# Kernel optimization log

Hardware: AMD Instinct MI355X
Metric: run time of the kernel (lower is better)

## Reference

```python
import jax, jax.numpy as jnp
import numpy as np
import math

B, S, D, H, L, K = 4, 2048, 256, 8, 2, 3  # batch, seq, dim, heads, MTA layers, conv kernel
HS = D // H
EPS = 1e-6


def layer_norm(x, g, b):
    m = jnp.mean(x, axis=-1, keepdims=True)
    v = jnp.mean((x - m) ** 2, axis=-1, keepdims=True)
    return (x - m) * jax.lax.rsqrt(v + EPS) * g + b


def temporal_encoder(x, W, b):
    # x: [B,S,D]; W: [L,K,D,D] (WIO), b: [L,D]. Stack of kernel-3 'SAME' Conv1d, GELU between.
    for i in range(L):
        x = jax.lax.conv_general_dilated(
            x, W[i], window_strides=(1,), padding=[(1, 1)],
            dimension_numbers=("NWC", "WIO", "NWC")) + b[i]
        if i < L - 1:
            x = jax.nn.gelu(x)
    return x


def setup_inputs() -> dict:
    key = jax.random.key(0)
    ks = jax.random.split(key, 10)
    w = lambda k, shape: jax.random.normal(k, shape, jnp.float32) * 0.02
    return {
        "x": jax.random.normal(ks[0], (B, S, D), jnp.float32),
        "ln1_g": jnp.ones((D,), jnp.float32), "ln1_b": jnp.zeros((D,), jnp.float32),
        "Wq": w(ks[1], (L, K, D, D)), "bq": jnp.zeros((L, D), jnp.float32),
        "Wk": w(ks[2], (L, K, D, D)), "bk": jnp.zeros((L, D), jnp.float32),
        "Wv": w(ks[3], (L, K, D, D)), "bv": jnp.zeros((L, D), jnp.float32),
        "ln2_g": jnp.ones((D,), jnp.float32), "ln2_b": jnp.zeros((D,), jnp.float32),
        "Wo1": w(ks[4], (D, D)), "bo1": jnp.zeros((D,), jnp.float32),
        "Wo2": w(ks[5], (D, D)), "bo2": jnp.zeros((D,), jnp.float32),
        "mask": jax.random.randint(ks[6], (B, S), 0, 2).astype(jnp.int32),
    }


def reference(x, ln1_g, ln1_b, Wq, bq, Wk, bk, Wv, bv, ln2_g, ln2_b, Wo1, bo1, Wo2, bo2, mask):
    b_, s_ = x.shape[0], x.shape[1]
    h = layer_norm(x, ln1_g, ln1_b)
    q = temporal_encoder(h, Wq, bq).reshape(b_, s_, H, HS)
    k = temporal_encoder(h, Wk, bk).reshape(b_, s_, H, HS)
    v = temporal_encoder(h, Wv, bv).reshape(b_, s_, H, HS)
    # attention scores [B,H,S,S]
    scores = jnp.einsum("bqhd,bkhd->bhqk", q, k) / math.sqrt(HS)
    m = mask[:, None, None, :].astype(scores.dtype)  # [B,1,1,S]
    scores = scores + (1.0 - m) * (-1e30)
    probs = jax.nn.softmax(scores, axis=-1)
    attn = jnp.einsum("bhqk,bkhd->bqhd", probs, v).reshape(b_, s_, D)
    residual = x + attn  # dropout p=0
    o = layer_norm(residual, ln2_g, ln2_b)
    o = jax.nn.gelu(o @ Wo1 + bo1)  # 1x1 Conv1D == per-token linear
    o = o @ Wo2 + bo2 + residual
    return o
```

## Files before the change

### kernel.cpp

```cpp
#include <hip/hip_runtime.h>
#include <hip/hip_bf16.h>
#include <math.h>

#define BB 4
#define SS 2048
#define DD 256
#define HH 8
#define HSZ 32

typedef __attribute__((ext_vector_type(8))) short short8;
typedef __attribute__((ext_vector_type(4))) float f32x4;

__device__ __forceinline__ void gload_lds16(const void* g, void* l) {
    __builtin_amdgcn_global_load_lds((const unsigned int*)g, (unsigned int*)l,
                                     16, 0, 0);
}

__device__ __forceinline__ float exp2_hw(float x) {
    float r;
    asm("v_exp_f32 %0, %1" : "=v"(r) : "v"(x));
    return r;
}

__device__ __forceinline__ unsigned int perm_pack(float a, float b, unsigned int sel) {
    unsigned int r;
    asm("v_perm_b32 %0, %1, %2, %3"
        : "=v"(r)
        : "v"(__float_as_uint(b)), "v"(__float_as_uint(a)), "s"(sel));
    return r;
}

__device__ __forceinline__ float gelu_f(float x) {
    float x3 = x * x * x;
    float z = 0.7978845608028654f * fmaf(0.044715f, x3, x);
    float e = __expf(2.0f * z);
    float t = 1.0f - 2.0f / (e + 1.0f);
    return 0.5f * x * (1.0f + t);
}

__device__ __forceinline__ unsigned short f2bf(float f) {
    unsigned int u = __float_as_uint(f);
    u = (u + 0x7fffu + ((u >> 16) & 1u)) >> 16;
    return (unsigned short)u;
}

template<bool HASRES>
__device__ __forceinline__ void ln_wave_body(
    int t, int lane,
    const float* __restrict__ x, const float* __restrict__ addin,
    const float* __restrict__ g, const float* __restrict__ bvec,
    float* __restrict__ resid_out, unsigned short* __restrict__ oln_bf)
{
    const int base = t * DD + lane * 4;
    float4 v4 = *(const float4*)&x[base];
    if (HASRES) {
        float4 a4 = *(const float4*)&addin[base];
        v4.x += a4.x; v4.y += a4.y; v4.z += a4.z; v4.w += a4.w;
        *(float4*)&resid_out[base] = v4;
    }
    float s = (v4.x + v4.y) + (v4.z + v4.w);
    #pragma unroll
    for (int o = 1; o < 64; o <<= 1) s += __shfl_xor(s, o);
    float mean = s * (1.0f / 256.0f);
    float dx = v4.x - mean, dy = v4.y - mean, dz = v4.z - mean, dw = v4.w - mean;
    float q = (dx * dx + dy * dy) + (dz * dz + dw * dw);
    #pragma unroll
    for (int o = 1; o < 64; o <<= 1) q += __shfl_xor(q, o);
    float r = rsqrtf(q * (1.0f / 256.0f) + 1e-6f);
    const float4 g4 = *(const float4*)&g[lane * 4];
    const float4 b4 = *(const float4*)&bvec[lane * 4];
    ushort4 o4;
    o4.x = f2bf(dx * r * g4.x + b4.x);
    o4.y = f2bf(dy * r * g4.y + b4.y);
    o4.z = f2bf(dz * r * g4.z + b4.z);
    o4.w = f2bf(dw * r * g4.w + b4.w);
    *(ushort4*)&oln_bf[base] = o4;
}

__global__ __launch_bounds__(256) void prep_kernel(
    const float* __restrict__ Wq, const float* __restrict__ Wk,
    const float* __restrict__ Wv, const float* __restrict__ Wo1,
    const float* __restrict__ Wo2, unsigned short* __restrict__ wt,
    const float* __restrict__ x, const float* __restrict__ ln1g,
    const float* __restrict__ ln1b, unsigned short* __restrict__ h_bf,
    const int* __restrict__ mask, float* __restrict__ maskf)
{
    if (blockIdx.x < 1280) {
        const int WCp = 3 * DD * DD;
        const int WMp = DD * DD;
        const float* src; unsigned short* dst; int R, rel;
        int i = blockIdx.x;
        if (i < 1152) {
            int seg = i / 192; rel = i % 192; R = 768;
            src = seg == 0 ? Wq : seg == 1 ? Wq + WCp : seg == 2 ? Wk :
                  seg == 3 ? Wk + WCp : seg == 4 ? Wv : Wv + WCp;
            dst = wt + (size_t)seg * WCp;
        } else {
            int j = i - 1152; int seg = j / 64; rel = j % 64; R = 256;
            src = seg == 0 ? Wo1 : Wo2;
            dst = wt + (size_t)6 * WCp + (size_t)seg * WMp;
        }
        __shared__ unsigned short t[32][33];
        const int tx = threadIdx.x & 31, ty = threadIdx.x >> 5;
        const int r0 = (rel / 8) * 32, c0 = (rel % 8) * 32;
        #pragma unroll
        for (int j = 0; j < 32; j += 8)
            t[ty + j][tx] = f2bf(src[(r0 + ty + j) * 256 + c0 + tx]);
        __syncthreads();
        #pragma unroll
        for (int j = 0; j < 32; j += 8)
            dst[(size_t)(c0 + ty + j) * R + r0 + tx] = t[tx][ty + j];
    } else if (blockIdx.x < 3328) {
        const int wv = threadIdx.x >> 6, lane = threadIdx.x & 63;
        ln_wave_body<false>((blockIdx.x - 1280) * 4 + wv, lane,
                            x, nullptr, ln1g, ln1b, nullptr, h_bf);
    } else {
        const float M_ON  = -8.0f * 1.4426950408889634f;
        const float M_OFF = -1.442695e30f;
        int i = (blockIdx.x - 3328) * 1024 + threadIdx.x * 4;
        int4 m4 = *(const int4*)&mask[i];
        float4 f4;
        f4.x = m4.x ? M_ON : M_OFF;
        f4.y = m4.y ? M_ON : M_OFF;
        f4.z = m4.z ? M_ON : M_OFF;
        f4.w = m4.w ? M_ON : M_OFF;
        *(float4*)&maskf[i] = f4;
    }
}

__global__ __launch_bounds__(256, 3) void convdual_kernel(
    const unsigned short* __restrict__ in,
    const unsigned short* __restrict__ W0a, const unsigned short* __restrict__ W0b,
    const unsigned short* __restrict__ W0c,
    const unsigned short* __restrict__ W1a, const unsigned short* __restrict__ W1b,
    const unsigned short* __restrict__ W1c,
    const float* __restrict__ ba, const float* __restrict__ bb,
    const float* __restrict__ bc,
    unsigned short* __restrict__ oQ, unsigned short* __restrict__ oK,
    unsigned short* __restrict__ oV, int S)
{
    constexpr int LDW = 264;
    __shared__ __align__(16) unsigned short stage[36 * LDW];
    __shared__ __align__(16) unsigned short wbuf[2][8192];

    unsigned short* const inter = stage;

    const int set = blockIdx.x % 3;
    const int tile = blockIdx.x / 3;
    const unsigned short* W0 = set == 0 ? W0a : (set == 1 ? W0b : W0c);
    const unsigned short* W1 = set == 0 ? W1a : (set == 1 ? W1b : W1c);
    const float* bias         = set == 0 ? ba  : (set == 1 ? bb  : bc);
    unsigned short* outp      = set == 0 ? oQ  : (set == 1 ? oK  : oV);

    const int tid = threadIdx.x;
    const int lane = tid & 63, wv = tid >> 6;
    const int lm = lane & 15, lq = lane >> 4;
    const int tpb = S / 32;
    const int b = tile / tpb;
    const int s0 = (tile % tpb) * 32;
    const int NC = S / 32;
    const int c = s0 >> 5;

    for (int i = tid; i < 36 * 32; i += 256) {
        int r = i >> 5, c8 = (i & 31) << 3;
        int s = s0 + r - 2;
        int4 val = make_int4(0, 0, 0, 0);
        if (s >= 0 && s < S)
            val = *(const int4*)&in[(size_t)(b * S + s) * 256 + c8];
        *(int4*)&stage[r * LDW + c8] = val;
    }

    const int n0 = wv * 64;

    const char* wsrc0[4];
    const char* wsrc1[4];
    char* wdst[4];
    {
        const unsigned int Lb = (unsigned int)(wv * 4096 + lane * 16);
        #pragma unroll
        for (int j = 0; j < 4; ++j) {
            unsigned int L = Lb + j * 1024u;
            unsigned int SL = L ^ (((L >> 7) & 7u) << 4);
            unsigned int so = (SL >> 6) * 1536u + (SL & 63u);
            wsrc0[j] = (const char*)W0 + so;
            wsrc1[j] = (const char*)W1 + so;
            wdst[j] = (char*)wbuf + (wv * 4096 + j * 1024);
        }
    }
    unsigned int boff[4];
    #pragma unroll
    for (int nt = 0; nt < 4; ++nt) {
        unsigned int och = (unsigned int)(n0 + nt * 16 + lm);
        unsigned int R = och * 64u + (unsigned int)lq * 16u;
        boff[nt] = R ^ (((R >> 7) & 7u) << 4);
    }

    __syncthreads();

    {
        f32x4 acc[3][4];
        #pragma unroll
        for (int mt = 0; mt < 3; ++mt)
            #pragma unroll
            for (int nt = 0; nt < 4; ++nt) acc[mt][nt] = (f32x4){0.f, 0.f, 0.f, 0.f};

        #pragma unroll
        for (int j = 0; j < 4; ++j) gload_lds16(wsrc0[j],       wdst[j]);
        #pragma unroll
        for (int j = 0; j < 4; ++j) gload_lds16(wsrc0[j] + 64,  wdst[j] + 16384);

        short8 a0c, a1c, a2c;
        {
            const int icc0 = lq * 8;
            int r20 = 32 + lm; r20 = r20 > 35 ? 35 : r20;
            a0c = *(const short8*)&stage[lm * LDW + icc0];
            a1c = *(const short8*)&stage[(16 + lm) * LDW + icc0];
            a2c = *(const short8*)&stage[r20 * LDW + icc0];
        }

        #pragma unroll
        for (int it = 0; it < 24; ++it) {
            if (it < 23) asm volatile("s_waitcnt vmcnt(4)" ::: "memory");
            else         asm volatile("s_waitcnt vmcnt(0)" ::: "memory");
            __builtin_amdgcn_sched_barrier(0);

            const char* wb = (const char*)wbuf + ((it & 1) << 14);
            short8 bfr[4];
            #pragma unroll
            for (int nt = 0; nt < 4; ++nt)
                bfr[nt] = *(const short8*)(wb + boff[nt]);

            short8 a0n, a1n, a2n;
            if (it + 1 < 24) {
                const int kk = (it + 1) >> 3;
                const int icc = ((it + 1) & 7) * 32 + lq * 8;
                int r2 = kk + 32 + lm; r2 = r2 > 35 ? 35 : r2;
                a0n = *(const short8*)&stage[(kk + lm) * LDW + icc];
                a1n = *(const short8*)&stage[(kk + 16 + lm) * LDW + icc];
                a2n = *(const short8*)&stage[r2 * LDW + icc];
            }

            __builtin_amdgcn_s_setprio(1);
            #pragma unroll
            for (int nt = 0; nt < 4; ++nt) {
                acc[0][nt] = __builtin_amdgcn_mfma_f32_16x16x32_bf16(a0c, bfr[nt], acc[0][nt], 0, 0, 0);
                acc[1][nt] = __builtin_amdgcn_mfma_f32_16x16x32_bf16(a1c, bfr[nt], acc[1][nt], 0, 0, 0);
                acc[2][nt] = __builtin_amdgcn_mfma_f32_16x16x32_bf16(a2c, bfr[nt], acc[2][nt], 0, 0, 0);
            }
            __builtin_amdgcn_s_setprio(0);
            __builtin_amdgcn_sched_barrier(0);

            if (it + 2 < 24) {
                char* ld = (char*)wbuf + ((it & 1) << 14);
                const int soff = (it + 2) * 64;
                #pragma unroll
                for (int j = 0; j < 4; ++j)
                    gload_lds16(wsrc0[j] + soff, ld + (wdst[j] - (char*)wbuf));
            }
            if (it + 1 < 24) { a0c = a0n; a1c = a1n; a2c = a2n; }
        }

        __syncthreads();

        #pragma unroll
        for (int mt = 0; mt < 3; ++mt)
            #pragma unroll
            for (int nt = 0; nt < 4; ++nt) {
                int ch = n0 + nt * 16 + lm;
                float bv = bias[ch];
                #pragma unroll
                for (int r = 0; r < 4; ++r) {
                    int j = mt * 16 + lq * 4 + r;
                    if (j < 34) {
                        int token = s0 - 1 + j;
                        unsigned short v = (token >= 0 && token < S)
                            ? f2bf(gelu_f(acc[mt][nt][r] + bv)) : (unsigned short)0;
                        inter[j * LDW + ch] = v;
                    }
                }
            }
    }
    __syncthreads();

    f32x4 acc2[2][4];
    #pragma unroll
    for (int mt = 0; mt < 2; ++mt)
        #pragma unroll
        for (int nt = 0; nt < 4; ++nt) acc2[mt][nt] = (f32x4){0.f, 0.f, 0.f, 0.f};
    {
        #pragma unroll
        for (int j = 0; j < 4; ++j) gload_lds16(wsrc1[j],       wdst[j]);
        #pragma unroll
        for (int j = 0; j < 4; ++j) gload_lds16(wsrc1[j] + 64,  wdst[j] + 16384);

        short8 a0c, a1c;
        {
            const int icc0 = lq * 8;
            a0c = *(const short8*)&inter[lm * LDW + icc0];
            a1c = *(const short8*)&inter[(16 + lm) * LDW + icc0];
        }

        #pragma unroll
        for (int it = 0; it < 24; ++it) {
            if (it < 23) asm volatile("s_waitcnt vmcnt(4)" ::: "memory");
            else         asm volatile("s_waitcnt vmcnt(0)" ::: "memory");
            __builtin_amdgcn_sched_barrier(0);

            const char* wb = (const char*)wbuf + ((it & 1) << 14);
            short8 bfr[4];
            #pragma unroll
            for (int nt = 0; nt < 4; ++nt)
                bfr[nt] = *(const short8*)(wb + boff[nt]);

            short8 a0n, a1n;
            if (it + 1 < 24) {
                const int kk = (it + 1) >> 3;
                const int icc = ((it + 1) & 7) * 32 + lq * 8;
                a0n = *(const short8*)&inter[(kk + lm) * LDW + icc];
                a1n = *(const short8*)&inter[(kk + 16 + lm) * LDW + icc];
            }

            __builtin_amdgcn_s_setprio(1);
            #pragma unroll
            for (int nt = 0; nt < 4; ++nt) {
                acc2[0][nt] = __builtin_amdgcn_mfma_f32_16x16x32_bf16(a0c, bfr[nt], acc2[0][nt], 0, 0, 0);
                acc2[1][nt] = __builtin_amdgcn_mfma_f32_16x16x32_bf16(a1c, bfr[nt], acc2[1][nt], 0, 0, 0);
            }
            __builtin_amdgcn_s_setprio(0);
            __builtin_amdgcn_sched_barrier(0);

            if (it + 2 < 24) {
                char* ld = (char*)wbuf + ((it & 1) << 14);
                const int soff = (it + 2) * 64;
                #pragma unroll
                for (int j = 0; j < 4; ++j)
                    gload_lds16(wsrc1[j] + soff, ld + (wdst[j] - (char*)wbuf));
            }
            if (it + 1 < 24) { a0c = a0n; a1c = a1n; }
        }
    }

    __syncthreads();
    if (set < 2) {
        #pragma unroll
        for (int mt = 0; mt < 2; ++mt)
            #pragma unroll
            for (int nt = 0; nt < 4; ++nt) {
                int o = n0 + nt * 16 + lm;
                int d = o & 31, h = o >> 5;
                float bv = bias[256 + o];
                #pragma unroll
                for (int r = 0; r < 4; ++r) {
                    int t = lq * 4 + r;
                    stage[mt * 4096 + (h * 64 + (d >> 3) * 16 + t) * 8 + (d & 7)] =
                        f2bf(acc2[mt][nt][r] + bv);
                }
            }
        __syncthreads();
        int h = tid >> 5;
        size_t base = ((size_t)(b * 8 + h) * NC + c) * 1024;
        #pragma unroll
        for (int half = 0; half < 2; ++half) {
            int4 v0 = *(const int4*)&stage[half * 4096 + tid * 16];
            int4 v1 = *(const int4*)&stage[half * 4096 + tid * 16 + 8];
            size_t dst = base + half * 512 + (tid & 31) * 16;
            *(int4*)&outp[dst] = v0;
            *(int4*)&outp[dst + 8] = v1;
        }
    } else {
        #pragma unroll
        for (int mt = 0; mt < 2; ++mt)
            #pragma unroll
            for (int nt = 0; nt < 4; ++nt) {
                int o = n0 + nt * 16 + lm;
                int d = o & 31, h = o >> 5;
                float bv = bias[256 + o];
                #pragma unroll
                for (int r = 0; r < 4; ++r) {
                    int t = lq * 4 + r;
                    stage[mt * 4096 +
                          ((h * 2 + (d >> 4)) * 32 + (t >> 3) * 16 + (d & 15)) * 8 + (t & 7)] =
                        f2bf(acc2[mt][nt][r] + bv);
                }
            }
        __syncthreads();
        int h = tid >> 5, dh = (tid >> 4) & 1;
        size_t base = ((size_t)(b * 8 + h) * NC + c) * 1024;
        #pragma unroll
        for (int half = 0; half < 2; ++half) {
            int4 v0 = *(const int4*)&stage[half * 4096 + tid * 16];
            int4 v1 = *(const int4*)&stage[half * 4096 + tid * 16 + 8];
            size_t dst = base + dh * 512 + half * 256 + (tid & 15) * 16;
            *(int4*)&outp[dst] = v0;
            *(int4*)&outp[dst + 8] = v1;
        }
    }
}

__global__ __launch_bounds__(256) void tail_kernel(
    const float* __restrict__ x, const float* __restrict__ attn,
    const float* __restrict__ g2, const float* __restrict__ b2,
    const unsigned short* __restrict__ W1, const float* __restrict__ bo1,
    const unsigned short* __restrict__ W2, const float* __restrict__ bo2,
    float* __restrict__ out, int S)
{
    constexpr int LDW = 264;
    __shared__ __align__(16) unsigned short h_lds[16 * LDW];
    __shared__ __align__(16) unsigned short h2_lds[16 * LDW];
    __shared__ __align__(16) float resid_lds[16][DD];

    const int tid = threadIdx.x;
    const int lane = tid & 63, wv = tid >> 6;
    const int lm = lane & 15, lq = lane >> 4;
    const int t0 = blockIdx.x * 16;

    #pragma unroll
    for (int j = 0; j < 4; ++j) {
        int t = wv * 4 + j;
        int base = (t0 + t) * DD + lane * 4;
        float4 v4 = *(const float4*)&x[base];
        float4 a4 = *(const float4*)&attn[base];
        v4.x += a4.x; v4.y += a4.y; v4.z += a4.z; v4.w += a4.w;
        *(float4*)&resid_lds[t][lane * 4] = v4;
        float s = (v4.x + v4.y) + (v4.z + v4.w);
        #pragma unroll
        for (int o = 1; o < 64; o <<= 1) s += __shfl_xor(s, o);
        float mean = s * (1.0f / 256.0f);
        float dx = v4.x - mean, dy = v4.y - mean, dz = v4.z - mean, dw = v4.w - mean;
        float q = (dx * dx + dy * dy) + (dz * dz + dw * dw);
        #pragma unroll
        for (int o = 1; o < 64; o <<= 1) q += __shfl_xor(q, o);
        float r = rsqrtf(q * (1.0f / 256.0f) + 1e-6f);
        const float4 g4 = *(const float4*)&g2[lane * 4];
        const float4 b4 = *(const float4*)&b2[lane * 4];
        ushort4 o4;
        o4.x = f2bf(dx * r * g4.x + b4.x);
        o4.y = f2bf(dy * r * g4.y + b4.y);
        o4.z = f2bf(dz * r * g4.z + b4.z);
        o4.w = f2bf(dw * r * g4.w + b4.w);
        *(ushort4*)&h_lds[t * LDW + lane * 4] = o4;
    }
    __syncthreads();

    const int n0 = wv * 64;

    {
        f32x4 acc[4];
        #pragma unroll
        for (int nt = 0; nt < 4; ++nt) acc[nt] = (f32x4){0.f, 0.f, 0.f, 0.f};
        const unsigned short* wp = W1 + (size_t)(n0 + lm) * 256 + lq * 8;
        short8 bf[4][4];
        #pragma unroll
        for (int p = 0; p < 3; ++p)
            #pragma unroll
            for (int nt = 0; nt < 4; ++nt)
                bf[p][nt] = *(const short8*)(wp + p * 32 + (size_t)nt * 16 * 256);
        #pragma unroll
        for (int it = 0; it < 8; ++it) {
            if (it + 3 < 8) {
                #pragma unroll
                for (int nt = 0; nt < 4; ++nt)
                    bf[(it + 3) & 3][nt] =
                        *(const short8*)(wp + (it + 3) * 32 + (size_t)nt * 16 * 256);
            }
            short8 a0 = *(const short8*)&h_lds[lm * LDW + it * 32 + lq * 8];
            #pragma unroll
            for (int nt = 0; nt < 4; ++nt)
                acc[nt] = __builtin_amdgcn_mfma_f32_16x16x32_bf16(a0, bf[it & 3][nt], acc[nt], 0, 0, 0);
        }
        #pragma unroll
        for (int nt = 0; nt < 4; ++nt) {
            int ch = n0 + nt * 16 + lm;
            float bv = bo1[ch];
            #pragma unroll
            for (int r = 0; r < 4; ++r) {
                int tok = lq * 4 + r;
                h2_lds[tok * LDW + ch] = f2bf(gelu_f(acc[nt][r] + bv));
            }
        }
    }
    __syncthreads();

    {
        f32x4 acc[4];
        #pragma unroll
        for (int nt = 0; nt < 4; ++nt) acc[nt] = (f32x4){0.f, 0.f, 0.f, 0.f};
        const unsigned short* wp = W2 + (size_t)(n0 + lm) * 256 + lq * 8;
        short8 bf[4][4];
        #pragma unroll
        for (int p = 0; p < 3; ++p)
            #pragma unroll
            for (int nt = 0; nt < 4; ++nt)
                bf[p][nt] = *(const short8*)(wp + p * 32 + (size_t)nt * 16 * 256);
        #pragma unroll
        for (int it = 0; it < 8; ++it) {
            if (it + 3 < 8) {
                #pragma unroll
                for (int nt = 0; nt < 4; ++nt)
                    bf[(it + 3) & 3][nt] =
                        *(const short8*)(wp + (it + 3) * 32 + (size_t)nt * 16 * 256);
            }
            short8 a0 = *(const short8*)&h2_lds[lm * LDW + it * 32 + lq * 8];
            #pragma unroll
            for (int nt = 0; nt < 4; ++nt)
                acc[nt] = __builtin_amdgcn_mfma_f32_16x16x32_bf16(a0, bf[it & 3][nt], acc[nt], 0, 0, 0);
        }
        #pragma unroll
        for (int nt = 0; nt < 4; ++nt) {
            int ch = n0 + nt * 16 + lm;
            float bv = bo2[ch];
            #pragma unroll
            for (int r = 0; r < 4; ++r) {
                int tok = lq * 4 + r;
                out[(size_t)(t0 + tok) * DD + ch] = acc[nt][r] + bv + resid_lds[tok][ch];
            }
        }
    }
}

__global__ __launch_bounds__(256) void attn_mfma_kernel(
    const unsigned short* __restrict__ Qf, const unsigned short* __restrict__ Kf,
    const unsigned short* __restrict__ Vf, const float* __restrict__ maskf,
    float* __restrict__ Out, int S, int H)
{
    constexpr int LDP = 40;
    __shared__ __align__(16) unsigned short p_lds[4][16 * LDP];

    const int bh = ((blockIdx.x & 7) << 2) | ((blockIdx.x >> 3) & 3);
    const int qt = (blockIdx.x >> 5) * 64;
    const int b = bh / H;
    const int tid = threadIdx.x;
    const int lane = tid & 63, wv = tid >> 6;
    const int lm = lane & 15, lq = lane >> 4;
    const int q0 = qt + wv * 16;
    const int NC = S / 32;

    const size_t base = (size_t)bh * NC * 1024;
    short8 qfrag = *(const short8*)&Qf[base + (size_t)(q0 >> 5) * 1024
                                      + ((q0 >> 4) & 1) * 512 + lane * 8];
    const unsigned short* kp = Kf + base + lane * 8;
    const unsigned short* vp = Vf + base + lane * 8;

    short8 ones;
    #pragma unroll
    for (int j = 0; j < 8; ++j) ones[j] = (short)0x3F80;

    f32x4 o0 = {0.f, 0.f, 0.f, 0.f}, o1 = {0.f, 0.f, 0.f, 0.f};
    const f32x4 zf = {0.f, 0.f, 0.f, 0.f};
    float l[4] = {0.f, 0.f, 0.f, 0.f};

    const float scale2 = 0.17677669529663687f * 1.4426950408889634f;
    const unsigned int psel = 0x07060302u;
    const float* mp0 = maskf + b * S + lq * 4;
    const float* mp1 = mp0 + 16;

    unsigned short* pw = p_lds[wv];
    const int pst = lm * LDP + lq * 4;
    const int prd = lm * LDP + lq * 8;

    short8 k0c = *(const short8*)(kp);
    short8 k1c = *(const short8*)(kp + 512);
    short8 v0c = *(const short8*)(vp);
    short8 v1c = *(const short8*)(vp + 512);

    #pragma unroll 2
    for (int c = 0; c < NC; ++c) {
        int cn = c + 1 < NC ? c + 1 : c;
        short8 k0n = *(const short8*)(kp + (size_t)cn * 1024);
        short8 k1n = *(const short8*)(kp + (size_t)cn * 1024 + 512);
        short8 v0n = *(const short8*)(vp + (size_t)cn * 1024);
        short8 v1n = *(const short8*)(vp + (size_t)cn * 1024 + 512);

        f32x4 s0 = __builtin_amdgcn_mfma_f32_16x16x32_bf16(k0c, qfrag, zf, 0, 0, 0);
        f32x4 s1 = __builtin_amdgcn_mfma_f32_16x16x32_bf16(k1c, qfrag, zf, 0, 0, 0);

        float4 mf0 = *(const float4*)(mp0 + c * 32);
        float4 mf1 = *(const float4*)(mp1 + c * 32);

        float p[8];
        p[0] = exp2_hw(fmaf(s0[0], scale2, mf0.x));
        p[1] = exp2_hw(fmaf(s0[1], scale2, mf0.y));
        p[2] = exp2_hw(fmaf(s0[2], scale2, mf0.z));
        p[3] = exp2_hw(fmaf(s0[3], scale2, mf0.w));
        p[4] = exp2_hw(fmaf(s1[0], scale2, mf1.x));
        p[5] = exp2_hw(fmaf(s1[1], scale2, mf1.y));
        p[6] = exp2_hw(fmaf(s1[2], scale2, mf1.z));
        p[7] = exp2_hw(fmaf(s1[3], scale2, mf1.w));

        uint2 w0, w1;
        w0.x = perm_pack(p[0], p[1], psel); w0.y = perm_pack(p[2], p[3], psel);
        w1.x = perm_pack(p[4], p[5], psel); w1.y = perm_pack(p[6], p[7], psel);
        *(uint2*)&pw[pst] = w0;
        *(uint2*)&pw[pst + 16] = w1;

        short8 pA = *(const short8*)&pw[prd];

        f32x4 lf = __builtin_amdgcn_mfma_f32_16x16x32_bf16(pA, ones, zf, 0, 0, 0);
        o0 = __builtin_amdgcn_mfma_f32_16x16x32_bf16(pA, v0c, o0, 0, 0, 0);
        o1 = __builtin_amdgcn_mfma_f32_16x16x32_bf16(pA, v1c, o1, 0, 0, 0);
        #pragma unroll
        for (int r = 0; r < 4; ++r) l[r] += lf[r];

        k0c = k0n; k1c = k1n; v0c = v0n; v1c = v1n;
    }

    #pragma unroll
    for (int r = 0; r < 4; ++r) {
        float inv = 1.0f / l[r];
        size_t ob = (size_t)(b * S + q0 + lq * 4 + r) * 256 + (bh % H) * 32;
        Out[ob + lm] = o0[r] * inv;
        Out[ob + 16 + lm] = o1[r] * inv;
    }
}

extern "C" void kernel_launch(void* const* d_in, const int* in_sizes, int n_in,
                              void* d_out, int out_size, void* d_ws, size_t ws_size,
                              hipStream_t stream) {
    (void)in_sizes; (void)n_in; (void)out_size; (void)ws_size;
    const float* x    = (const float*)d_in[0];
    const float* ln1g = (const float*)d_in[1];
    const float* ln1b = (const float*)d_in[2];
    const float* Wq   = (const float*)d_in[3];
    const float* bq   = (const float*)d_in[4];
    const float* Wk   = (const float*)d_in[5];
    const float* bk   = (const float*)d_in[6];
    const float* Wv   = (const float*)d_in[7];
    const float* bv   = (const float*)d_in[8];
    const float* ln2g = (const float*)d_in[9];
    const float* ln2b = (const float*)d_in[10];
    const float* Wo1  = (const float*)d_in[11];
    const float* bo1  = (const float*)d_in[12];
    const float* Wo2  = (const float*)d_in[13];
    const float* bo2  = (const float*)d_in[14];
    const int*   mask = (const int*)d_in[15];
    float* out = (float*)d_out;

    const int S = SS, H = HH;
    const int T = BB * SS;
    const size_t NE = (size_t)T * DD;
    float* ws    = (float*)d_ws;
    float* attn  = ws + 0 * NE;
    float* maskf = ws + 1 * NE;
    unsigned short* qf_g  = (unsigned short*)(ws + 2 * NE);
    unsigned short* kf_g  = qf_g + NE;
    unsigned short* h_bf  = kf_g + NE;
    unsigned short* wt    = h_bf + NE;
    const int WC = 3 * DD * DD;
    const int WM = DD * DD;
    unsigned short* wtq0 = wt;
    unsigned short* wtq1 = wt + WC;
    unsigned short* wtk0 = wt + 2 * WC;
    unsigned short* wtk1 = wt + 3 * WC;
    unsigned short* wtv0 = wt + 4 * WC;
    unsigned short* wtv1 = wt + 5 * WC;
    unsigned short* wto1 = wt + 6 * WC;
    unsigned short* wto2 = wt + 6 * WC + WM;
    unsigned short* vf_g = wt + 6 * WC + 2 * WM;

    prep_kernel<<<1280 + T / 4 + 8, 256, 0, stream>>>(
        Wq, Wk, Wv, Wo1, Wo2, wt, x, ln1g, ln1b, h_bf, mask, maskf);

    convdual_kernel<<<(T / 32) * 3, 256, 0, stream>>>(
        h_bf, wtq0, wtk0, wtv0, wtq1, wtk1, wtv1, bq, bk, bv,
        qf_g, kf_g, vf_g, S);

    attn_mfma_kernel<<<BB * H * (S / 64), 256, 0, stream>>>(qf_g, kf_g, vf_g, maskf, attn, S, H);

    tail_kernel<<<T / 16, 256, 0, stream>>>(
        x, attn, ln2g, ln2b, wto1, bo1, wto2, bo2, out, S);
}
```

Measured before the change: 213.0 us.

## Software-pipeline weight LDS reads and stream tail weights through LDS

In the conv kernel, the B-fragment LDS reads for the next iteration are issued before the current MFMAs, so LDS latency overlaps the matrix math. The second layer's weight prefetch now starts before the GELU epilogue of the first layer. The tail kernel is changed to stage W1/W2 through double-buffered LDS with async global-to-LDS loads instead of direct global register loads, and gets a 2-blocks-per-CU launch bound. Waiting on vmcnt(0) every iteration may serialize loads more than the previous vmcnt(4), and the extra 32KB of LDS may limit tail-kernel occupancy.

```diff
diff --git a/kernel.cpp b/kernel.cpp
--- a/kernel.cpp
+++ b/kernel.cpp
@@ -205,9 +205,9 @@
             for (int nt = 0; nt < 4; ++nt) acc[mt][nt] = (f32x4){0.f, 0.f, 0.f, 0.f};
 
         #pragma unroll
-        for (int j = 0; j < 4; ++j) gload_lds16(wsrc0[j],       wdst[j]);
-        #pragma unroll
-        for (int j = 0; j < 4; ++j) gload_lds16(wsrc0[j] + 64,  wdst[j] + 16384);
+        for (int j = 0; j < 4; ++j) gload_lds16(wsrc0[j],      wdst[j]);
+        #pragma unroll
+        for (int j = 0; j < 4; ++j) gload_lds16(wsrc0[j] + 64, wdst[j] + 16384);
 
         short8 a0c, a1c, a2c;
         {
@@ -218,20 +218,26 @@
             a2c = *(const short8*)&stage[r20 * LDW + icc0];
         }
 
+        asm volatile("s_waitcnt vmcnt(4)" ::: "memory");
+        __builtin_amdgcn_sched_barrier(0);
+        short8 bfc[4];
+        #pragma unroll
+        for (int nt = 0; nt < 4; ++nt)
+            bfc[nt] = *(const short8*)((const char*)wbuf + boff[nt]);
+        asm volatile("s_waitcnt lgkmcnt(0)" ::: "memory");
+        __builtin_amdgcn_sched_barrier(0);
+
         #pragma unroll
         for (int it = 0; it < 24; ++it) {
-            if (it < 23) asm volatile("s_waitcnt vmcnt(4)" ::: "memory");
-            else         asm volatile("s_waitcnt vmcnt(0)" ::: "memory");
-            __builtin_amdgcn_sched_barrier(0);
-
-            const char* wb = (const char*)wbuf + ((it & 1) << 14);
-            short8 bfr[4];
-            #pragma unroll
-            for (int nt = 0; nt < 4; ++nt)
-                bfr[nt] = *(const short8*)(wb + boff[nt]);
-
+            short8 bfn[4];
             short8 a0n, a1n, a2n;
             if (it + 1 < 24) {
+                asm volatile("s_waitcnt vmcnt(0)" ::: "memory");
+                __builtin_amdgcn_sched_barrier(0);
+                const char* wb = (const char*)wbuf + (((it + 1) & 1) << 14);
+                #pragma unroll
+                for (int nt = 0; nt < 4; ++nt)
+                    bfn[nt] = *(const short8*)(wb + boff[nt]);
                 const int kk = (it + 1) >> 3;
                 const int icc = ((it + 1) & 7) * 32 + lq * 8;
                 int r2 = kk + 32 + lm; r2 = r2 > 35 ? 35 : r2;
@@ -239,17 +245,6 @@
                 a1n = *(const short8*)&stage[(kk + 16 + lm) * LDW + icc];
                 a2n = *(const short8*)&stage[r2 * LDW + icc];
             }
-
-            __builtin_amdgcn_s_setprio(1);
-            #pragma unroll
-            for (int nt = 0; nt < 4; ++nt) {
-                acc[0][nt] = __builtin_amdgcn_mfma_f32_16x16x32_bf16(a0c, bfr[nt], acc[0][nt], 0, 0, 0);
-                acc[1][nt] = __builtin_amdgcn_mfma_f32_16x16x32_bf16(a1c, bfr[nt], acc[1][nt], 0, 0, 0);
-                acc[2][nt] = __builtin_amdgcn_mfma_f32_16x16x32_bf16(a2c, bfr[nt], acc[2][nt], 0, 0, 0);
-            }
-            __builtin_amdgcn_s_setprio(0);
-            __builtin_amdgcn_sched_barrier(0);
-
             if (it + 2 < 24) {
                 char* ld = (char*)wbuf + ((it & 1) << 14);
                 const int soff = (it + 2) * 64;
@@ -257,10 +252,27 @@
                 for (int j = 0; j < 4; ++j)
                     gload_lds16(wsrc0[j] + soff, ld + (wdst[j] - (char*)wbuf));
             }
-            if (it + 1 < 24) { a0c = a0n; a1c = a1n; a2c = a2n; }
+            __builtin_amdgcn_s_setprio(1);
+            #pragma unroll
+            for (int nt = 0; nt < 4; ++nt) {
+                acc[0][nt] = __builtin_amdgcn_mfma_f32_16x16x32_bf16(a0c, bfc[nt], acc[0][nt], 0, 0, 0);
+                acc[1][nt] = __builtin_amdgcn_mfma_f32_16x16x32_bf16(a1c, bfc[nt], acc[1][nt], 0, 0, 0);
+                acc[2][nt] = __builtin_amdgcn_mfma_f32_16x16x32_bf16(a2c, bfc[nt], acc[2][nt], 0, 0, 0);
+            }
+            __builtin_amdgcn_s_setprio(0);
+            if (it + 1 < 24) {
+                #pragma unroll
+                for (int nt = 0; nt < 4; ++nt) bfc[nt] = bfn[nt];
+                a0c = a0n; a1c = a1n; a2c = a2n;
+            }
         }
 
         __syncthreads();
+
+        #pragma unroll
+        for (int j = 0; j < 4; ++j) gload_lds16(wsrc1[j],      wdst[j]);
+        #pragma unroll
+        for (int j = 0; j < 4; ++j) gload_lds16(wsrc1[j] + 64, wdst[j] + 16384);
 
         #pragma unroll
         for (int mt = 0; mt < 3; ++mt)
@@ -288,11 +300,6 @@
         #pragma unroll
         for (int nt = 0; nt < 4; ++nt) acc2[mt][nt] = (f32x4){0.f, 0.f, 0.f, 0.f};
     {
-        #pragma unroll
-        for (int j = 0; j < 4; ++j) gload_lds16(wsrc1[j],       wdst[j]);
-        #pragma unroll
-        for (int j = 0; j < 4; ++j) gload_lds16(wsrc1[j] + 64,  wdst[j] + 16384);
-
         short8 a0c, a1c;
         {
             const int icc0 = lq * 8;
@@ -300,35 +307,31 @@
             a1c = *(const short8*)&inter[(16 + lm) * LDW + icc0];
         }
 
+        asm volatile("s_waitcnt vmcnt(4)" ::: "memory");
+        __builtin_amdgcn_sched_barrier(0);
+        short8 bfc[4];
+        #pragma unroll
+        for (int nt = 0; nt < 4; ++nt)
+            bfc[nt] = *(const short8*)((const char*)wbuf + boff[nt]);
+        asm volatile("s_waitcnt lgkmcnt(0)" ::: "memory");
+        __builtin_amdgcn_sched_barrier(0);
+
         #pragma unroll
         for (int it = 0; it < 24; ++it) {
-            if (it < 23) asm volatile("s_waitcnt vmcnt(4)" ::: "memory");
-            else         asm volatile("s_waitcnt vmcnt(0)" ::: "memory");
-            __builtin_amdgcn_sched_barrier(0);
-
-            const char* wb = (const char*)wbuf + ((it & 1) << 14);
-            short8 bfr[4];
-            #pragma unroll
-            for (int nt = 0; nt < 4; ++nt)
-                bfr[nt] = *(const short8*)(wb + boff[nt]);
-
+            short8 bfn[4];
             short8 a0n, a1n;
             if (it + 1 < 24) {
+                asm volatile("s_waitcnt vmcnt(0)" ::: "memory");
+                __builtin_amdgcn_sched_barrier(0);
+                const char* wb = (const char*)wbuf + (((it + 1) & 1) << 14);
+                #pragma unroll
+                for (int nt = 0; nt < 4; ++nt)
+                    bfn[nt] = *(const short8*)(wb + boff[nt]);
                 const int kk = (it + 1) >> 3;
                 const int icc = ((it + 1) & 7) * 32 + lq * 8;
                 a0n = *(const short8*)&inter[(kk + lm) * LDW + icc];
                 a1n = *(const short8*)&inter[(kk + 16 + lm) * LDW + icc];
             }
-
-            __builtin_amdgcn_s_setprio(1);
-            #pragma unroll
-            for (int nt = 0; nt < 4; ++nt) {
-                acc2[0][nt] = __builtin_amdgcn_mfma_f32_16x16x32_bf16(a0c, bfr[nt], acc2[0][nt], 0, 0, 0);
-                acc2[1][nt] = __builtin_amdgcn_mfma_f32_16x16x32_bf16(a1c, bfr[nt], acc2[1][nt], 0, 0, 0);
-            }
-            __builtin_amdgcn_s_setprio(0);
-            __builtin_amdgcn_sched_barrier(0);
-
             if (it + 2 < 24) {
                 char* ld = (char*)wbuf + ((it & 1) << 14);
                 const int soff = (it + 2) * 64;
@@ -336,7 +339,18 @@
                 for (int j = 0; j < 4; ++j)
                     gload_lds16(wsrc1[j] + soff, ld + (wdst[j] - (char*)wbuf));
             }
-            if (it + 1 < 24) { a0c = a0n; a1c = a1n; }
+            __builtin_amdgcn_s_setprio(1);
+            #pragma unroll
+            for (int nt = 0; nt < 4; ++nt) {
+                acc2[0][nt] = __builtin_amdgcn_mfma_f32_16x16x32_bf16(a0c, bfc[nt], acc2[0][nt], 0, 0, 0);
+                acc2[1][nt] = __builtin_amdgcn_mfma_f32_16x16x32_bf16(a1c, bfc[nt], acc2[1][nt], 0, 0, 0);
+            }
+            __builtin_amdgcn_s_setprio(0);
+            if (it + 1 < 24) {
+                #pragma unroll
+                for (int nt = 0; nt < 4; ++nt) bfc[nt] = bfn[nt];
+                a0c = a0n; a1c = a1n;
+            }
         }
     }
 
@@ -397,7 +411,7 @@
     }
 }
 
-__global__ __launch_bounds__(256) void tail_kernel(
+__global__ __launch_bounds__(256, 2) void tail_kernel(
     const float* __restrict__ x, const float* __restrict__ attn,
     const float* __restrict__ g2, const float* __restrict__ b2,
     const unsigned short* __restrict__ W1, const float* __restrict__ bo1,
@@ -408,11 +422,41 @@
     __shared__ __align__(16) unsigned short h_lds[16 * LDW];
     __shared__ __align__(16) unsigned short h2_lds[16 * LDW];
     __shared__ __align__(16) float resid_lds[16][DD];
+    __shared__ __align__(16) unsigned short wbuf[2][8192];
 
     const int tid = threadIdx.x;
     const int lane = tid & 63, wv = tid >> 6;
     const int lm = lane & 15, lq = lane >> 4;
     const int t0 = blockIdx.x * 16;
+    const int n0 = wv * 64;
+
+    const char* wsrc1[4];
+    const char* wsrc2[4];
+    char* wdst[4];
+    {
+        const unsigned int Lb = (unsigned int)(wv * 4096 + lane * 16);
+        #pragma unroll
+        for (int j = 0; j < 4; ++j) {
+            unsigned int L = Lb + j * 1024u;
+            unsigned int SL = L ^ (((L >> 7) & 7u) << 4);
+            unsigned int so = (SL >> 6) * 512u + (SL & 63u);
+            wsrc1[j] = (const char*)W1 + so;
+            wsrc2[j] = (const char*)W2 + so;
+            wdst[j] = (char*)wbuf + (wv * 4096 + j * 1024);
+        }
+    }
+    unsigned int boff[4];
+    #pragma unroll
+    for (int nt = 0; nt < 4; ++nt) {
+        unsigned int och = (unsigned int)(n0 + nt * 16 + lm);
+        unsigned int R = och * 64u + (unsigned int)lq * 16u;
+        boff[nt] = R ^ (((R >> 7) & 7u) << 4);
+    }
+
+    #pragma unroll
+    for (int j = 0; j < 4; ++j) gload_lds16(wsrc1[j],      wdst[j]);
+    #pragma unroll
+    for (int j = 0; j < 4; ++j) gload_lds16(wsrc1[j] + 64, wdst[j] + 16384);
 
     #pragma unroll
     for (int j = 0; j < 4; ++j) {
@@ -442,32 +486,57 @@
     }
     __syncthreads();
 
-    const int n0 = wv * 64;
-
     {
         f32x4 acc[4];
         #pragma unroll
         for (int nt = 0; nt < 4; ++nt) acc[nt] = (f32x4){0.f, 0.f, 0.f, 0.f};
-        const unsigned short* wp = W1 + (size_t)(n0 + lm) * 256 + lq * 8;
-        short8 bf[4][4];
-        #pragma unroll
-        for (int p = 0; p < 3; ++p)
+
+        short8 a0c = *(const short8*)&h_lds[lm * LDW + lq * 8];
+        asm volatile("s_waitcnt vmcnt(4)" ::: "memory");
+        __builtin_amdgcn_sched_barrier(0);
+        short8 bfc[4];
+        #pragma unroll
+        for (int nt = 0; nt < 4; ++nt)
+            bfc[nt] = *(const short8*)((const char*)wbuf + boff[nt]);
+        asm volatile("s_waitcnt lgkmcnt(0)" ::: "memory");
+        __builtin_amdgcn_sched_barrier(0);
+
+        #pragma unroll
+        for (int it = 0; it < 8; ++it) {
+            short8 bfn[4], a0n;
+            if (it + 1 < 8) {
+                asm volatile("s_waitcnt vmcnt(0)" ::: "memory");
+                __builtin_amdgcn_sched_barrier(0);
+                const char* wb = (const char*)wbuf + (((it + 1) & 1) << 14);
+                #pragma unroll
+                for (int nt = 0; nt < 4; ++nt)
+                    bfn[nt] = *(const short8*)(wb + boff[nt]);
+                a0n = *(const short8*)&h_lds[lm * LDW + (it + 1) * 32 + lq * 8];
+            }
+            if (it + 2 < 8) {
+                char* ld = (char*)wbuf + ((it & 1) << 14);
+                const int soff = (it + 2) * 64;
+                #pragma unroll
+                for (int j = 0; j < 4; ++j)
+                    gload_lds16(wsrc1[j] + soff, ld + (wdst[j] - (char*)wbuf));
+            }
+            __builtin_amdgcn_s_setprio(1);
             #pragma unroll
             for (int nt = 0; nt < 4; ++nt)
-                bf[p][nt] = *(const short8*)(wp + p * 32 + (size_t)nt * 16 * 256);
-        #pragma unroll
-        for (int it = 0; it < 8; ++it) {
-            if (it + 3 < 8) {
-                #pragma unroll
-                for (int nt = 0; nt < 4; ++nt)
-                    bf[(it + 3) & 3][nt] =
-                        *(const short8*)(wp + (it + 3) * 32 + (size_t)nt * 16 * 256);
-            }
-            short8 a0 = *(const short8*)&h_lds[lm * LDW + it * 32 + lq * 8];
-            #pragma unroll
-            for (int nt = 0; nt < 4; ++nt)
-                acc[nt] = __builtin_amdgcn_mfma_f32_16x16x32_bf16(a0, bf[it & 3][nt], acc[nt], 0, 0, 0);
-        }
+                acc[nt] = __builtin_amdgcn_mfma_f32_16x16x32_bf16(a0c, bfc[nt], acc[nt], 0, 0, 0);
+            __builtin_amdgcn_s_setprio(0);
+            if (it + 1 < 8) {
+                #pragma unroll
+                for (int nt = 0; nt < 4; ++nt) bfc[nt] = bfn[nt];
+                a0c = a0n;
+            }
+        }
+
+        #pragma unroll
+        for (int j = 0; j < 4; ++j) gload_lds16(wsrc2[j],      wdst[j]);
+        #pragma unroll
+        for (int j = 0; j < 4; ++j) gload_lds16(wsrc2[j] + 64, wdst[j] + 16384);
+
         #pragma unroll
         for (int nt = 0; nt < 4; ++nt) {
             int ch = n0 + nt * 16 + lm;
@@ -485,25 +554,46 @@
         f32x4 acc[4];
         #pragma unroll
         for (int nt = 0; nt < 4; ++nt) acc[nt] = (f32x4){0.f, 0.f, 0.f, 0.f};
-        const unsigned short* wp = W2 + (size_t)(n0 + lm) * 256 + lq * 8;
-        short8 bf[4][4];
-        #pragma unroll
-        for (int p = 0; p < 3; ++p)
+
+        short8 a0c = *(const short8*)&h2_lds[lm * LDW + lq * 8];
+        asm volatile("s_waitcnt vmcnt(4)" ::: "memory");
+        __builtin_amdgcn_sched_barrier(0);
+        short8 bfc[4];
+        #pragma unroll
+        for (int nt = 0; nt < 4; ++nt)
+            bfc[nt] = *(const short8*)((const char*)wbuf + boff[nt]);
+        asm volatile("s_waitcnt lgkmcnt(0)" ::: "memory");
+        __builtin_amdgcn_sched_barrier(0);
+
+        #pragma unroll
+        for (int it = 0; it < 8; ++it) {
+            short8 bfn[4], a0n;
+            if (it + 1 < 8) {
+                asm volatile("s_waitcnt vmcnt(0)" ::: "memory");
+                __builtin_amdgcn_sched_barrier(0);
+                const char* wb = (const char*)wbuf + (((it + 1) & 1) << 14);
+                #pragma unroll
+                for (int nt = 0; nt < 4; ++nt)
+                    bfn[nt] = *(const short8*)(wb + boff[nt]);
+                a0n = *(const short8*)&h2_lds[lm * LDW + (it + 1) * 32 + lq * 8];
+            }
+            if (it + 2 < 8) {
+                char* ld = (char*)wbuf + ((it & 1) << 14);
+                const int soff = (it + 2) * 64;
+                #pragma unroll
+                for (int j = 0; j < 4; ++j)
+                    gload_lds16(wsrc2[j] + soff, ld + (wdst[j] - (char*)wbuf));
+            }
+            __builtin_amdgcn_s_setprio(1);
             #pragma unroll
             for (int nt = 0; nt < 4; ++nt)
-                bf[p][nt] = *(const short8*)(wp + p * 32 + (size_t)nt * 16 * 256);
-        #pragma unroll
-        for (int it = 0; it < 8; ++it) {
-            if (it + 3 < 8) {
-                #pragma unroll
-                for (int nt = 0; nt < 4; ++nt)
-                    bf[(it + 3) & 3][nt] =
-                        *(const short8*)(wp + (it + 3) * 32 + (size_t)nt * 16 * 256);
-            }
-            short8 a0 = *(const short8*)&h2_lds[lm * LDW + it * 32 + lq * 8];
-            #pragma unroll
-            for (int nt = 0; nt < 4; ++nt)
-                acc[nt] = __builtin_amdgcn_mfma_f32_16x16x32_bf16(a0, bf[it & 3][nt], acc[nt], 0, 0, 0);
+                acc[nt] = __builtin_amdgcn_mfma_f32_16x16x32_bf16(a0c, bfc[nt], acc[nt], 0, 0, 0);
+            __builtin_amdgcn_s_setprio(0);
+            if (it + 1 < 8) {
+                #pragma unroll
+                for (int nt = 0; nt < 4; ++nt) bfc[nt] = bfn[nt];
+                a0c = a0n;
+            }
         }
         #pragma unroll
         for (int nt = 0; nt < 4; ++nt) {
```

After: 203.1 us. -4.6%, faster.
